# Performance work log

Hardware: AMD Instinct MI355X
Metric: run time of the kernel (lower is better)

Reference implementation:

```python
import jax, jax.numpy as jnp
import numpy as np

N_EMBD = 64
HEAD_SIZE = 64
BLOCK_SIZE = 256


def setup_inputs() -> dict:
    key = jax.random.key(0)
    ks = jax.random.split(key, 7)
    B, T = 1024, 256
    inputs = jax.random.normal(ks[0], (B, T, N_EMBD), dtype=jnp.float32)
    s = 1.0 / np.sqrt(N_EMBD)
    Wq = jax.random.uniform(ks[1], (HEAD_SIZE, N_EMBD), jnp.float32, -s, s)
    Wk = jax.random.uniform(ks[2], (HEAD_SIZE, N_EMBD), jnp.float32, -s, s)
    Wv = jax.random.uniform(ks[3], (HEAD_SIZE, N_EMBD), jnp.float32, -s, s)
    bq = jax.random.uniform(ks[4], (HEAD_SIZE,), jnp.float32, -s, s)
    bk = jax.random.uniform(ks[5], (HEAD_SIZE,), jnp.float32, -s, s)
    bv = jax.random.uniform(ks[6], (HEAD_SIZE,), jnp.float32, -s, s)
    return {"inputs": inputs, "Wq": Wq, "bq": bq, "Wk": Wk, "bk": bk, "Wv": Wv, "bv": bv}


def reference(inputs, Wq, bq, Wk, bk, Wv, bv):
    # inputs: [B, T, C]; Linear weights stored torch-style [out, in]
    T = inputs.shape[1]
    Q = jnp.einsum('btc,hc->bth', inputs, Wq) + bq  # [B,T,H]
    K = jnp.einsum('btc,hc->bth', inputs, Wk) + bk
    V = jnp.einsum('btc,hc->bth', inputs, Wv) + bv
    scale = 1.0 / jnp.sqrt(jnp.float32(K.shape[-1]))
    scores = jnp.einsum('bth,bsh->bts', Q, K) * scale  # [B,T,T]
    causal = jnp.triu(jnp.ones((T, T), dtype=bool), k=1)
    scores = jnp.where(causal, jnp.float32(-1e9), scores)
    attn = jax.nn.softmax(scores, axis=-1)
    return jnp.einsum('bts,bsh->bth', attn, V)
```

## Files before the change

kernel.cpp:

```cpp
#include <hip/hip_runtime.h>

typedef __attribute__((ext_vector_type(8))) __bf16 bf16x8;
typedef __attribute__((ext_vector_type(4))) float f32x4;
typedef __attribute__((ext_vector_type(4))) unsigned int u32x4;
typedef __attribute__((ext_vector_type(2))) unsigned int u32x2;

#define LDS_SCR 0
#define LDS_K   10240
#define LDS_VT  43008
#define LDS_TOT 75776
#define W_Q (LDS_VT)
#define W_K (LDS_VT + 8192)
#define W_V (LDS_VT + 16384)

#define QSCALE 0.180336880f

static __device__ __forceinline__ float exp2g(float x) {
#if __has_builtin(__builtin_amdgcn_exp2f)
  return __builtin_amdgcn_exp2f(x);
#else
  return exp2f(x);
#endif
}
static __device__ __forceinline__ unsigned int cvt_pk_bf16(float a, float b) {
  unsigned int r;
  asm("v_cvt_pk_bf16_f32 %0, %1, %2" : "=v"(r) : "v"(a), "v"(b));
  return r;
}
static __device__ __forceinline__ int swz128(int row, int colbyte) {
  return row * 128 + (colbyte ^ ((row & 7) << 4));
}
static __device__ __forceinline__ int swz512(int row, int colbyte) {
  return row * 512 + (colbyte ^ ((row & 7) << 4));
}
static __device__ __forceinline__ bf16x8 ldx(const float* p) {
  const float4* p4 = (const float4*)p;
  float4 lo = p4[0], hi = p4[1];
  u32x4 u;
  u.x = cvt_pk_bf16(lo.x, lo.y); u.y = cvt_pk_bf16(lo.z, lo.w);
  u.z = cvt_pk_bf16(hi.x, hi.y); u.w = cvt_pk_bf16(hi.z, hi.w);
  return __builtin_bit_cast(bf16x8, u);
}

static __device__ __forceinline__ void qk_unit(const char* smemK, int ln, int g,
    bf16x8 q0, bf16x8 q1, int jt, f32x4 (&s)[4])
{
#pragma unroll
  for (int nk = 0; nk < 4; ++nk) s[nk] = (f32x4){0.f, 0.f, 0.f, 0.f};
  __builtin_amdgcn_s_setprio(1);
#pragma unroll
  for (int ks = 0; ks < 2; ++ks) {
    bf16x8 qk = ks ? q1 : q0;
    bf16x8 kb[4];
#pragma unroll
    for (int nk = 0; nk < 4; ++nk) {
      u32x4 u = *(const u32x4*)(smemK + swz128(jt * 64 + nk * 16 + ln, (ks * 32 + g * 8) * 2));
      kb[nk] = __builtin_bit_cast(bf16x8, u);
    }
#pragma unroll
    for (int nk = 0; nk < 4; ++nk)
      s[nk] = __builtin_amdgcn_mfma_f32_16x16x32_bf16(kb[nk], qk, s[nk], 0, 0, 0);
  }
  __builtin_amdgcn_s_setprio(0);
}
static __device__ __forceinline__ void exp_unit(f32x4 (&s)[4], float& lpart)
{
  float sum = 0.f;
#pragma unroll
  for (int nk = 0; nk < 4; ++nk)
#pragma unroll
    for (int d = 0; d < 4; ++d) {
      float p = exp2g(s[nk][d]);
      s[nk][d] = p;
      sum += p;
    }
  lpart += sum;
}
static __device__ __forceinline__ void pv_half(char* scr, const char* smemVT, int ln, int g,
    int jt, int h2, const f32x4& sa, const f32x4& sb, f32x4 (&oacc)[4])
{
  {
    u32x2 p;
    p.x = cvt_pk_bf16(sa[0], sa[1]); p.y = cvt_pk_bf16(sa[2], sa[3]);
    *(u32x2*)(scr + ln * 80 + 0 * 32 + g * 8) = p;
  }
  {
    u32x2 p;
    p.x = cvt_pk_bf16(sb[0], sb[1]); p.y = cvt_pk_bf16(sb[2], sb[3]);
    *(u32x2*)(scr + ln * 80 + 1 * 32 + g * 8) = p;
  }
  bf16x8 pa;
  {
    u32x4 u = *(const u32x4*)(scr + ln * 80 + g * 16);
    pa = __builtin_bit_cast(bf16x8, u);
  }
  bf16x8 vb[4];
#pragma unroll
  for (int nf = 0; nf < 4; ++nf) {
    int key0 = jt * 64 + h2 * 32 + g * 8;
    u32x4 u = *(const u32x4*)(smemVT + swz512(nf * 16 + ln, key0 * 2));
    vb[nf] = __builtin_bit_cast(bf16x8, u);
  }
  __builtin_amdgcn_s_setprio(1);
#pragma unroll
  for (int nf = 0; nf < 4; ++nf)
    oacc[nf] = __builtin_amdgcn_mfma_f32_16x16x32_bf16(pa, vb[nf], oacc[nf], 0, 0, 0);
  __builtin_amdgcn_s_setprio(0);
}
static __device__ __forceinline__ void epi_unit(float* og, f32x4 (&oacc)[4], float lpart,
                                                int qbase, int ln, int g)
{
  float lsum = lpart;
  lsum += __shfl_xor(lsum, 16);
  lsum += __shfl_xor(lsum, 32);
  float linv = 1.0f / lsum;
  float inv[4];
#pragma unroll
  for (int d = 0; d < 4; ++d) inv[d] = __shfl(linv, g * 4 + d);
#pragma unroll
  for (int nf = 0; nf < 4; ++nf)
#pragma unroll
    for (int d = 0; d < 4; ++d) {
      int t = qbase + g * 4 + d;
      og[t * 64 + nf * 16 + ln] = oacc[nf][d] * inv[d];
    }
}

__global__ __launch_bounds__(512, 4)
void head_fused(const float* __restrict__ x,
                const float* __restrict__ Wq, const float* __restrict__ bq,
                const float* __restrict__ Wk, const float* __restrict__ bk,
                const float* __restrict__ Wv, const float* __restrict__ bv,
                float* __restrict__ out)
{
  __shared__ __align__(16) char smem[LDS_TOT];
  const int b    = blockIdx.x;
  const int tid  = threadIdx.x;
  const int lane = tid & 63;
  const int wid  = tid >> 6;
  const int g    = lane >> 4;
  const int ln   = lane & 15;
  const int tA   = wid;
  const int tB   = 15 - wid;

  const float* xb = x + (size_t)b * (256 * 64);
  char* scr = smem + LDS_SCR + wid * 1280;

  bf16x8 xfA[2], xfB[2];
#pragma unroll
  for (int ks = 0; ks < 2; ++ks) {
    xfA[ks] = ldx(xb + (tA * 16 + ln) * 64 + ks * 32 + g * 8);
    xfB[ks] = ldx(xb + (tB * 16 + ln) * 64 + ks * 32 + g * 8);
  }

#pragma unroll
  for (int i = 0; i < 6; ++i) {
    int idx = tid + i * 512;
    int mat = idx >> 10;
    int rem = idx & 1023;
    const float4* wg = (const float4*)(mat == 0 ? Wq : (mat == 1 ? Wk : Wv));
    float4 v = wg[rem];
    int e = rem * 4;
    int h = e >> 6, c = e & 63;
    u32x2 p;
    p.x = cvt_pk_bf16(v.x, v.y);
    p.y = cvt_pk_bf16(v.z, v.w);
    *(u32x2*)(smem + W_Q + mat * 8192 + swz128(h, c * 2)) = p;
  }
  __syncthreads();

  bf16x8 qaA[2], qaB[2];
#pragma unroll
  for (int ti = 0; ti < 2; ++ti) {
    bf16x8 xf0 = ti ? xfB[0] : xfA[0];
    bf16x8 xf1 = ti ? xfB[1] : xfA[1];
#pragma unroll
    for (int hk = 0; hk < 2; ++hk) {
#pragma unroll
      for (int mt2 = 0; mt2 < 2; ++mt2) {
        int mt = hk * 2 + mt2;
        float4 bb = *(const float4*)(bq + mt * 16 + g * 4);
        f32x4 acc = {0.f, 0.f, 0.f, 0.f};
        {
          u32x4 u = *(const u32x4*)(smem + W_Q + swz128(mt * 16 + ln, (0 * 32 + g * 8) * 2));
          acc = __builtin_amdgcn_mfma_f32_16x16x32_bf16(__builtin_bit_cast(bf16x8, u), xf0, acc, 0, 0, 0);
        }
        {
          u32x4 u = *(const u32x4*)(smem + W_Q + swz128(mt * 16 + ln, (1 * 32 + g * 8) * 2));
          acc = __builtin_amdgcn_mfma_f32_16x16x32_bf16(__builtin_bit_cast(bf16x8, u), xf1, acc, 0, 0, 0);
        }
        u32x2 p;
        p.x = cvt_pk_bf16((acc[0] + bb.x) * QSCALE, (acc[1] + bb.y) * QSCALE);
        p.y = cvt_pk_bf16((acc[2] + bb.z) * QSCALE, (acc[3] + bb.w) * QSCALE);
        *(u32x2*)(scr + ln * 80 + mt2 * 32 + g * 8) = p;
      }
      u32x4 u = *(const u32x4*)(scr + ln * 80 + g * 16);
      if (ti) qaB[hk] = __builtin_bit_cast(bf16x8, u);
      else    qaA[hk] = __builtin_bit_cast(bf16x8, u);
    }
  }

#pragma unroll
  for (int ti = 0; ti < 2; ++ti) {
    int tile = ti ? tB : tA;
    bf16x8 xf0 = ti ? xfB[0] : xfA[0];
    bf16x8 xf1 = ti ? xfB[1] : xfA[1];
#pragma unroll
    for (int mt = 0; mt < 4; ++mt) {
      float4 bb = *(const float4*)(bk + mt * 16 + g * 4);
      f32x4 acc = {0.f, 0.f, 0.f, 0.f};
      {
        u32x4 u = *(const u32x4*)(smem + W_K + swz128(mt * 16 + ln, (0 * 32 + g * 8) * 2));
        acc = __builtin_amdgcn_mfma_f32_16x16x32_bf16(__builtin_bit_cast(bf16x8, u), xf0, acc, 0, 0, 0);
      }
      {
        u32x4 u = *(const u32x4*)(smem + W_K + swz128(mt * 16 + ln, (1 * 32 + g * 8) * 2));
        acc = __builtin_amdgcn_mfma_f32_16x16x32_bf16(__builtin_bit_cast(bf16x8, u), xf1, acc, 0, 0, 0);
      }
      u32x2 p;
      p.x = cvt_pk_bf16(acc[0] + bb.x, acc[1] + bb.y);
      p.y = cvt_pk_bf16(acc[2] + bb.z, acc[3] + bb.w);
      *(u32x2*)(smem + LDS_K + swz128(tile * 16 + ln, (mt * 16 + g * 4) * 2)) = p;
    }
  }

  bf16x8 wv[4][2];
  float bvv[4];
#pragma unroll
  for (int nf = 0; nf < 4; ++nf) {
    bvv[nf] = bv[nf * 16 + ln];
#pragma unroll
    for (int ks = 0; ks < 2; ++ks) {
      u32x4 u = *(const u32x4*)(smem + W_V + swz128(nf * 16 + ln, (ks * 32 + g * 8) * 2));
      wv[nf][ks] = __builtin_bit_cast(bf16x8, u);
    }
  }
  __syncthreads();

#pragma unroll
  for (int ti = 0; ti < 2; ++ti) {
    int tile = ti ? tB : tA;
    bf16x8 xf0 = ti ? xfB[0] : xfA[0];
    bf16x8 xf1 = ti ? xfB[1] : xfA[1];
#pragma unroll
    for (int nf = 0; nf < 4; ++nf) {
      f32x4 acc = {0.f, 0.f, 0.f, 0.f};
      acc = __builtin_amdgcn_mfma_f32_16x16x32_bf16(xf0, wv[nf][0], acc, 0, 0, 0);
      acc = __builtin_amdgcn_mfma_f32_16x16x32_bf16(xf1, wv[nf][1], acc, 0, 0, 0);
      int t0 = tile * 16 + g * 4;
      u32x2 p;
      p.x = cvt_pk_bf16(acc[0] + bvv[nf], acc[1] + bvv[nf]);
      p.y = cvt_pk_bf16(acc[2] + bvv[nf], acc[3] + bvv[nf]);
      *(u32x2*)(smem + LDS_VT + swz512(nf * 16 + ln, t0 * 2)) = p;
    }
  }
  __syncthreads();

  float* og = out + (size_t)b * (256 * 64);
  const char* smemK  = smem + LDS_K;
  const char* smemVT = smem + LDS_VT;

#pragma unroll
  for (int ti = 0; ti < 2; ++ti) {
    const int tile = ti ? tB : tA;
    bf16x8 qa0 = ti ? qaB[0] : qaA[0];
    bf16x8 qa1 = ti ? qaB[1] : qaA[1];
    const int qbase = tile * 16;
    const int jmaxT = qbase >> 6;
    const int t3    = tile & 3;

    float lpart = 0.f;
    f32x4 oacc[4];
#pragma unroll
    for (int nf = 0; nf < 4; ++nf)
      oacc[nf] = (f32x4){0.f, 0.f, 0.f, 0.f};
    f32x4 s[4];

    for (int jt = 0; jt < jmaxT; ++jt) {
      qk_unit(smemK, ln, g, qa0, qa1, jt, s);
      exp_unit(s, lpart);
      pv_half(scr, smemVT, ln, g, jt, 0, s[0], s[1], oacc);
      pv_half(scr, smemVT, ln, g, jt, 1, s[2], s[3], oacc);
    }

    {
      const int jt = jmaxT;
#pragma unroll
      for (int nk = 0; nk < 4; ++nk) s[nk] = (f32x4){0.f, 0.f, 0.f, 0.f};
      __builtin_amdgcn_s_setprio(1);
#pragma unroll
      for (int ks = 0; ks < 2; ++ks) {
        bf16x8 qk = ks ? qa1 : qa0;
#pragma unroll
        for (int nk = 0; nk < 4; ++nk) {
          if (nk <= t3) {
            u32x4 u = *(const u32x4*)(smemK + swz128(jt * 64 + nk * 16 + ln, (ks * 32 + g * 8) * 2));
            s[nk] = __builtin_amdgcn_mfma_f32_16x16x32_bf16(
                      __builtin_bit_cast(bf16x8, u), qk, s[nk], 0, 0, 0);
          }
        }
      }
      __builtin_amdgcn_s_setprio(0);
#pragma unroll
      for (int nk = 0; nk < 4; ++nk) {
        if (nk == t3) {
#pragma unroll
          for (int d = 0; d < 4; ++d)
            s[nk][d] = (g * 4 + d > ln) ? -1e30f : s[nk][d];
        }
      }
      {
        float sum = 0.f;
#pragma unroll
        for (int nk = 0; nk < 4; ++nk) {
          if (nk <= t3) {
#pragma unroll
            for (int d = 0; d < 4; ++d) {
              float p = exp2g(s[nk][d]);
              s[nk][d] = p;
              sum += p;
            }
          }
        }
        lpart += sum;
      }
      pv_half(scr, smemVT, ln, g, jt, 0, s[0], s[1], oacc);
      if (t3 >= 2)
        pv_half(scr, smemVT, ln, g, jt, 1, s[2], s[3], oacc);
    }

    epi_unit(og, oacc, lpart, qbase, ln, g);
  }
}

extern "C" void kernel_launch(void* const* d_in, const int* in_sizes, int n_in,
                              void* d_out, int out_size, void* d_ws, size_t ws_size,
                              hipStream_t stream) {
  (void)in_sizes; (void)n_in; (void)d_ws; (void)ws_size; (void)out_size;
  const float* x  = (const float*)d_in[0];
  const float* Wq = (const float*)d_in[1];
  const float* bq = (const float*)d_in[2];
  const float* Wk = (const float*)d_in[3];
  const float* bk = (const float*)d_in[4];
  const float* Wv = (const float*)d_in[5];
  const float* bv = (const float*)d_in[6];
  float* out = (float*)d_out;
  hipLaunchKernelGGL(head_fused, dim3(1024), dim3(512), 0, stream,
                     x, Wq, bq, Wk, bk, Wv, bv, out);
}
```

Before: 38.26 us.

## Process two batches per persistent block, keeping converted weights resident in LDS

Halves the grid so each block loops over two batch elements. The Q/K/V weights are converted to bf16 once into a dedicated LDS region and reused for both batches, where before they were staged in the V^T area and overwritten. This is meant to amortise the per-block weight load and conversion and the launch tail. In exchange, LDS per block grows from about 74 KB to about 98 KB, which may reduce how many blocks fit per CU. The second batch also adds a barrier before K is overwritten and runs serially within each block.

```diff
diff --git a/kernel.cpp b/kernel.cpp
--- a/kernel.cpp
+++ b/kernel.cpp
@@ -8,10 +8,10 @@
 #define LDS_SCR 0
 #define LDS_K   10240
 #define LDS_VT  43008
-#define LDS_TOT 75776
-#define W_Q (LDS_VT)
-#define W_K (LDS_VT + 8192)
-#define W_V (LDS_VT + 16384)
+#define W_Q     75776
+#define W_K     83968
+#define W_V     92160
+#define LDS_TOT 100352
 
 #define QSCALE 0.180336880f
 
@@ -134,7 +134,6 @@
                 float* __restrict__ out)
 {
   __shared__ __align__(16) char smem[LDS_TOT];
-  const int b    = blockIdx.x;
   const int tid  = threadIdx.x;
   const int lane = tid & 63;
   const int wid  = tid >> 6;
@@ -143,15 +142,9 @@
   const int tA   = wid;
   const int tB   = 15 - wid;
 
-  const float* xb = x + (size_t)b * (256 * 64);
   char* scr = smem + LDS_SCR + wid * 1280;
-
-  bf16x8 xfA[2], xfB[2];
-#pragma unroll
-  for (int ks = 0; ks < 2; ++ks) {
-    xfA[ks] = ldx(xb + (tA * 16 + ln) * 64 + ks * 32 + g * 8);
-    xfB[ks] = ldx(xb + (tB * 16 + ln) * 64 + ks * 32 + g * 8);
-  }
+  const char* smemK  = smem + LDS_K;
+  const char* smemVT = smem + LDS_VT;
 
 #pragma unroll
   for (int i = 0; i < 6; ++i) {
@@ -169,167 +162,173 @@
   }
   __syncthreads();
 
-  bf16x8 qaA[2], qaB[2];
-#pragma unroll
-  for (int ti = 0; ti < 2; ++ti) {
-    bf16x8 xf0 = ti ? xfB[0] : xfA[0];
-    bf16x8 xf1 = ti ? xfB[1] : xfA[1];
-#pragma unroll
-    for (int hk = 0; hk < 2; ++hk) {
-#pragma unroll
-      for (int mt2 = 0; mt2 < 2; ++mt2) {
-        int mt = hk * 2 + mt2;
-        float4 bb = *(const float4*)(bq + mt * 16 + g * 4);
+#pragma unroll 1
+  for (int bi = 0; bi < 2; ++bi) {
+    const int bb = blockIdx.x + bi * 512;
+    const float* xb = x + (size_t)bb * (256 * 64);
+    float* og = out + (size_t)bb * (256 * 64);
+
+    bf16x8 xfA[2], xfB[2];
+#pragma unroll
+    for (int ks = 0; ks < 2; ++ks) {
+      xfA[ks] = ldx(xb + (tA * 16 + ln) * 64 + ks * 32 + g * 8);
+      xfB[ks] = ldx(xb + (tB * 16 + ln) * 64 + ks * 32 + g * 8);
+    }
+
+    bf16x8 qaA[2], qaB[2];
+#pragma unroll
+    for (int ti = 0; ti < 2; ++ti) {
+      bf16x8 xf0 = ti ? xfB[0] : xfA[0];
+      bf16x8 xf1 = ti ? xfB[1] : xfA[1];
+#pragma unroll
+      for (int hk = 0; hk < 2; ++hk) {
+#pragma unroll
+        for (int mt2 = 0; mt2 < 2; ++mt2) {
+          int mt = hk * 2 + mt2;
+          float4 bb4 = *(const float4*)(bq + mt * 16 + g * 4);
+          f32x4 acc = {0.f, 0.f, 0.f, 0.f};
+          {
+            u32x4 u = *(const u32x4*)(smem + W_Q + swz128(mt * 16 + ln, (0 * 32 + g * 8) * 2));
+            acc = __builtin_amdgcn_mfma_f32_16x16x32_bf16(__builtin_bit_cast(bf16x8, u), xf0, acc, 0, 0, 0);
+          }
+          {
+            u32x4 u = *(const u32x4*)(smem + W_Q + swz128(mt * 16 + ln, (1 * 32 + g * 8) * 2));
+            acc = __builtin_amdgcn_mfma_f32_16x16x32_bf16(__builtin_bit_cast(bf16x8, u), xf1, acc, 0, 0, 0);
+          }
+          u32x2 p;
+          p.x = cvt_pk_bf16((acc[0] + bb4.x) * QSCALE, (acc[1] + bb4.y) * QSCALE);
+          p.y = cvt_pk_bf16((acc[2] + bb4.z) * QSCALE, (acc[3] + bb4.w) * QSCALE);
+          *(u32x2*)(scr + ln * 80 + mt2 * 32 + g * 8) = p;
+        }
+        u32x4 u = *(const u32x4*)(scr + ln * 80 + g * 16);
+        if (ti) qaB[hk] = __builtin_bit_cast(bf16x8, u);
+        else    qaA[hk] = __builtin_bit_cast(bf16x8, u);
+      }
+    }
+
+    if (bi) __syncthreads();
+
+#pragma unroll
+    for (int ti = 0; ti < 2; ++ti) {
+      int tile = ti ? tB : tA;
+      bf16x8 xf0 = ti ? xfB[0] : xfA[0];
+      bf16x8 xf1 = ti ? xfB[1] : xfA[1];
+#pragma unroll
+      for (int mt = 0; mt < 4; ++mt) {
+        float4 bb4 = *(const float4*)(bk + mt * 16 + g * 4);
         f32x4 acc = {0.f, 0.f, 0.f, 0.f};
         {
-          u32x4 u = *(const u32x4*)(smem + W_Q + swz128(mt * 16 + ln, (0 * 32 + g * 8) * 2));
+          u32x4 u = *(const u32x4*)(smem + W_K + swz128(mt * 16 + ln, (0 * 32 + g * 8) * 2));
           acc = __builtin_amdgcn_mfma_f32_16x16x32_bf16(__builtin_bit_cast(bf16x8, u), xf0, acc, 0, 0, 0);
         }
         {
-          u32x4 u = *(const u32x4*)(smem + W_Q + swz128(mt * 16 + ln, (1 * 32 + g * 8) * 2));
+          u32x4 u = *(const u32x4*)(smem + W_K + swz128(mt * 16 + ln, (1 * 32 + g * 8) * 2));
           acc = __builtin_amdgcn_mfma_f32_16x16x32_bf16(__builtin_bit_cast(bf16x8, u), xf1, acc, 0, 0, 0);
         }
         u32x2 p;
-        p.x = cvt_pk_bf16((acc[0] + bb.x) * QSCALE, (acc[1] + bb.y) * QSCALE);
-        p.y = cvt_pk_bf16((acc[2] + bb.z) * QSCALE, (acc[3] + bb.w) * QSCALE);
-        *(u32x2*)(scr + ln * 80 + mt2 * 32 + g * 8) = p;
-      }
-      u32x4 u = *(const u32x4*)(scr + ln * 80 + g * 16);
-      if (ti) qaB[hk] = __builtin_bit_cast(bf16x8, u);
-      else    qaA[hk] = __builtin_bit_cast(bf16x8, u);
-    }
-  }
-
-#pragma unroll
-  for (int ti = 0; ti < 2; ++ti) {
-    int tile = ti ? tB : tA;
-    bf16x8 xf0 = ti ? xfB[0] : xfA[0];
-    bf16x8 xf1 = ti ? xfB[1] : xfA[1];
-#pragma unroll
-    for (int mt = 0; mt < 4; ++mt) {
-      float4 bb = *(const float4*)(bk + mt * 16 + g * 4);
-      f32x4 acc = {0.f, 0.f, 0.f, 0.f};
+        p.x = cvt_pk_bf16(acc[0] + bb4.x, acc[1] + bb4.y);
+        p.y = cvt_pk_bf16(acc[2] + bb4.z, acc[3] + bb4.w);
+        *(u32x2*)(smem + LDS_K + swz128(tile * 16 + ln, (mt * 16 + g * 4) * 2)) = p;
+      }
+    }
+
+#pragma unroll
+    for (int ti = 0; ti < 2; ++ti) {
+      int tile = ti ? tB : tA;
+      bf16x8 xf0 = ti ? xfB[0] : xfA[0];
+      bf16x8 xf1 = ti ? xfB[1] : xfA[1];
+#pragma unroll
+      for (int nf = 0; nf < 4; ++nf) {
+        float bvv = bv[nf * 16 + ln];
+        f32x4 acc = {0.f, 0.f, 0.f, 0.f};
+        {
+          u32x4 u = *(const u32x4*)(smem + W_V + swz128(nf * 16 + ln, (0 * 32 + g * 8) * 2));
+          acc = __builtin_amdgcn_mfma_f32_16x16x32_bf16(xf0, __builtin_bit_cast(bf16x8, u), acc, 0, 0, 0);
+        }
+        {
+          u32x4 u = *(const u32x4*)(smem + W_V + swz128(nf * 16 + ln, (1 * 32 + g * 8) * 2));
+          acc = __builtin_amdgcn_mfma_f32_16x16x32_bf16(xf1, __builtin_bit_cast(bf16x8, u), acc, 0, 0, 0);
+        }
+        int t0 = tile * 16 + g * 4;
+        u32x2 p;
+        p.x = cvt_pk_bf16(acc[0] + bvv, acc[1] + bvv);
+        p.y = cvt_pk_bf16(acc[2] + bvv, acc[3] + bvv);
+        *(u32x2*)(smem + LDS_VT + swz512(nf * 16 + ln, t0 * 2)) = p;
+      }
+    }
+    __syncthreads();
+
+#pragma unroll
+    for (int ti = 0; ti < 2; ++ti) {
+      const int tile = ti ? tB : tA;
+      bf16x8 qa0 = ti ? qaB[0] : qaA[0];
+      bf16x8 qa1 = ti ? qaB[1] : qaA[1];
+      const int qbase = tile * 16;
+      const int jmaxT = qbase >> 6;
+      const int t3    = tile & 3;
+
+      float lpart = 0.f;
+      f32x4 oacc[4];
+#pragma unroll
+      for (int nf = 0; nf < 4; ++nf)
+        oacc[nf] = (f32x4){0.f, 0.f, 0.f, 0.f};
+      f32x4 s[4];
+
+      for (int jt = 0; jt < jmaxT; ++jt) {
+        qk_unit(smemK, ln, g, qa0, qa1, jt, s);
+        exp_unit(s, lpart);
+        pv_half(scr, smemVT, ln, g, jt, 0, s[0], s[1], oacc);
+        pv_half(scr, smemVT, ln, g, jt, 1, s[2], s[3], oacc);
+      }
+
       {
-        u32x4 u = *(const u32x4*)(smem + W_K + swz128(mt * 16 + ln, (0 * 32 + g * 8) * 2));
-        acc = __builtin_amdgcn_mfma_f32_16x16x32_bf16(__builtin_bit_cast(bf16x8, u), xf0, acc, 0, 0, 0);
-      }
-      {
-        u32x4 u = *(const u32x4*)(smem + W_K + swz128(mt * 16 + ln, (1 * 32 + g * 8) * 2));
-        acc = __builtin_amdgcn_mfma_f32_16x16x32_bf16(__builtin_bit_cast(bf16x8, u), xf1, acc, 0, 0, 0);
-      }
-      u32x2 p;
-      p.x = cvt_pk_bf16(acc[0] + bb.x, acc[1] + bb.y);
-      p.y = cvt_pk_bf16(acc[2] + bb.z, acc[3] + bb.w);
-      *(u32x2*)(smem + LDS_K + swz128(tile * 16 + ln, (mt * 16 + g * 4) * 2)) = p;
-    }
-  }
-
-  bf16x8 wv[4][2];
-  float bvv[4];
-#pragma unroll
-  for (int nf = 0; nf < 4; ++nf) {
-    bvv[nf] = bv[nf * 16 + ln];
-#pragma unroll
-    for (int ks = 0; ks < 2; ++ks) {
-      u32x4 u = *(const u32x4*)(smem + W_V + swz128(nf * 16 + ln, (ks * 32 + g * 8) * 2));
-      wv[nf][ks] = __builtin_bit_cast(bf16x8, u);
-    }
-  }
-  __syncthreads();
-
-#pragma unroll
-  for (int ti = 0; ti < 2; ++ti) {
-    int tile = ti ? tB : tA;
-    bf16x8 xf0 = ti ? xfB[0] : xfA[0];
-    bf16x8 xf1 = ti ? xfB[1] : xfA[1];
-#pragma unroll
-    for (int nf = 0; nf < 4; ++nf) {
-      f32x4 acc = {0.f, 0.f, 0.f, 0.f};
-      acc = __builtin_amdgcn_mfma_f32_16x16x32_bf16(xf0, wv[nf][0], acc, 0, 0, 0);
-      acc = __builtin_amdgcn_mfma_f32_16x16x32_bf16(xf1, wv[nf][1], acc, 0, 0, 0);
-      int t0 = tile * 16 + g * 4;
-      u32x2 p;
-      p.x = cvt_pk_bf16(acc[0] + bvv[nf], acc[1] + bvv[nf]);
-      p.y = cvt_pk_bf16(acc[2] + bvv[nf], acc[3] + bvv[nf]);
-      *(u32x2*)(smem + LDS_VT + swz512(nf * 16 + ln, t0 * 2)) = p;
-    }
-  }
-  __syncthreads();
-
-  float* og = out + (size_t)b * (256 * 64);
-  const char* smemK  = smem + LDS_K;
-  const char* smemVT = smem + LDS_VT;
-
-#pragma unroll
-  for (int ti = 0; ti < 2; ++ti) {
-    const int tile = ti ? tB : tA;
-    bf16x8 qa0 = ti ? qaB[0] : qaA[0];
-    bf16x8 qa1 = ti ? qaB[1] : qaA[1];
-    const int qbase = tile * 16;
-    const int jmaxT = qbase >> 6;
-    const int t3    = tile & 3;
-
-    float lpart = 0.f;
-    f32x4 oacc[4];
-#pragma unroll
-    for (int nf = 0; nf < 4; ++nf)
-      oacc[nf] = (f32x4){0.f, 0.f, 0.f, 0.f};
-    f32x4 s[4];
-
-    for (int jt = 0; jt < jmaxT; ++jt) {
-      qk_unit(smemK, ln, g, qa0, qa1, jt, s);
-      exp_unit(s, lpart);
-      pv_half(scr, smemVT, ln, g, jt, 0, s[0], s[1], oacc);
-      pv_half(scr, smemVT, ln, g, jt, 1, s[2], s[3], oacc);
-    }
-
-    {
-      const int jt = jmaxT;
-#pragma unroll
-      for (int nk = 0; nk < 4; ++nk) s[nk] = (f32x4){0.f, 0.f, 0.f, 0.f};
-      __builtin_amdgcn_s_setprio(1);
-#pragma unroll
-      for (int ks = 0; ks < 2; ++ks) {
-        bf16x8 qk = ks ? qa1 : qa0;
+        const int jt = jmaxT;
+#pragma unroll
+        for (int nk = 0; nk < 4; ++nk) s[nk] = (f32x4){0.f, 0.f, 0.f, 0.f};
+        __builtin_amdgcn_s_setprio(1);
+#pragma unroll
+        for (int ks = 0; ks < 2; ++ks) {
+          bf16x8 qk = ks ? qa1 : qa0;
+#pragma unroll
+          for (int nk = 0; nk < 4; ++nk) {
+            if (nk <= t3) {
+              u32x4 u = *(const u32x4*)(smemK + swz128(jt * 64 + nk * 16 + ln, (ks * 32 + g * 8) * 2));
+              s[nk] = __builtin_amdgcn_mfma_f32_16x16x32_bf16(
+                        __builtin_bit_cast(bf16x8, u), qk, s[nk], 0, 0, 0);
+            }
+          }
+        }
+        __builtin_amdgcn_s_setprio(0);
 #pragma unroll
         for (int nk = 0; nk < 4; ++nk) {
-          if (nk <= t3) {
-            u32x4 u = *(const u32x4*)(smemK + swz128(jt * 64 + nk * 16 + ln, (ks * 32 + g * 8) * 2));
-            s[nk] = __builtin_amdgcn_mfma_f32_16x16x32_bf16(
-                      __builtin_bit_cast(bf16x8, u), qk, s[nk], 0, 0, 0);
-          }
-        }
-      }
-      __builtin_amdgcn_s_setprio(0);
-#pragma unroll
-      for (int nk = 0; nk < 4; ++nk) {
-        if (nk == t3) {
-#pragma unroll
-          for (int d = 0; d < 4; ++d)
-            s[nk][d] = (g * 4 + d > ln) ? -1e30f : s[nk][d];
-        }
-      }
-      {
-        float sum = 0.f;
-#pragma unroll
-        for (int nk = 0; nk < 4; ++nk) {
-          if (nk <= t3) {
-#pragma unroll
-            for (int d = 0; d < 4; ++d) {
-              float p = exp2g(s[nk][d]);
-              s[nk][d] = p;
-              sum += p;
+          if (nk == t3) {
+#pragma unroll
+            for (int d = 0; d < 4; ++d)
+              s[nk][d] = (g * 4 + d > ln) ? -1e30f : s[nk][d];
+          }
+        }
+        {
+          float sum = 0.f;
+#pragma unroll
+          for (int nk = 0; nk < 4; ++nk) {
+            if (nk <= t3) {
+#pragma unroll
+              for (int d = 0; d < 4; ++d) {
+                float p = exp2g(s[nk][d]);
+                s[nk][d] = p;
+                sum += p;
+              }
             }
           }
-        }
-        lpart += sum;
-      }
-      pv_half(scr, smemVT, ln, g, jt, 0, s[0], s[1], oacc);
-      if (t3 >= 2)
-        pv_half(scr, smemVT, ln, g, jt, 1, s[2], s[3], oacc);
-    }
-
-    epi_unit(og, oacc, lpart, qbase, ln, g);
+          lpart += sum;
+        }
+        pv_half(scr, smemVT, ln, g, jt, 0, s[0], s[1], oacc);
+        if (t3 >= 2)
+          pv_half(scr, smemVT, ln, g, jt, 1, s[2], s[3], oacc);
+      }
+
+      epi_unit(og, oacc, lpart, qbase, ln, g);
+    }
   }
 }
 
@@ -345,6 +344,6 @@
   const float* Wv = (const float*)d_in[5];
   const float* bv = (const float*)d_in[6];
   float* out = (float*)d_out;
-  hipLaunchKernelGGL(head_fused, dim3(1024), dim3(512), 0, stream,
+  hipLaunchKernelGGL(head_fused, dim3(512), dim3(512), 0, stream,
                      x, Wq, bq, Wk, bk, Wv, bv, out);
 }
```

New measurement: 45.99 us. 20.2% more time.
